# Performance work log

Hardware: AMD Instinct MI355X
Metric: run time of the kernel (lower is better)

## Reference

```python
import jax, jax.numpy as jnp
import numpy as np
from jax import lax

B, T, D, V, K = 32, 2048, 512, 1024, 3
COVERAGE_FLOOR = 0.05
LN_EPS = 1e-5


def _gelu(x):
    return jax.nn.gelu(x, approximate=False)  # torch F.gelu default is exact erf


def _causal_conv(h, w, b):
    # h: [B,T,D]; w: [D_out, D_in, K]; left-pad (K-1) for causality
    x = jnp.transpose(h, (0, 2, 1))  # [B,D,T]
    y = lax.conv_general_dilated(x, w, window_strides=(1,),
                                 padding=[(w.shape[-1] - 1, 0)],
                                 dimension_numbers=("NCH", "OIH", "NCH"))
    return jnp.transpose(y + b[None, :, None], (0, 2, 1))  # [B,T,D]


def _layer_norm(x, g, b):
    m = x.mean(-1, keepdims=True)
    v = ((x - m) ** 2).mean(-1, keepdims=True)
    return (x - m) / jnp.sqrt(v + LN_EPS) * g + b


def _masked_median(values, mask):
    # values, mask: [B,T]; torch median = lower middle = sorted[(n-1)//2]
    valid = mask > 0.5
    n = valid.sum(axis=1)  # [B]
    s = jnp.sort(jnp.where(valid, values, jnp.inf), axis=1)
    idx = jnp.clip((n - 1) // 2, 0, values.shape[1] - 1)
    med = jnp.take_along_axis(s, idx[:, None], axis=1)  # [B,1]
    return jnp.where((n > 0)[:, None], med, 0.0)


def _masked_mean(values, mask):
    denom = jnp.clip(mask.sum(axis=1, keepdims=True), 1.0, None)  # [B,1]
    return (values * mask[:, :, None]).sum(axis=1) / denom  # [B,D]


def _masked_std(values, mask, mean):
    denom = jnp.clip(mask.sum(axis=1, keepdims=True), 1.0, None)
    diff2 = (values - mean[:, None, :]) ** 2 * mask[:, :, None]
    return jnp.sqrt(diff2.sum(axis=1) / jnp.clip(denom, 1e-6, None) + 1e-6)


def setup_inputs() -> dict:
    key = jax.random.key(0)
    ks = jax.random.split(key, 16)
    s = 0.02
    return {
        "unit_ids": jax.random.randint(ks[0], (B, T), 0, V),
        "duration_obs": jax.random.uniform(ks[1], (B, T), jnp.float32, 0.01, 2.0),
        "mask": (jax.random.uniform(ks[2], (B, T)) > 0.3).astype(jnp.float32),
        "emb": jax.random.normal(ks[3], (V, D), jnp.float32) * s,
        "aux_w": jax.random.normal(ks[4], (D, 1), jnp.float32) * s,
        "aux_b": jnp.zeros((D,), jnp.float32),
        "conv1_w": jax.random.normal(ks[5], (D, D, K), jnp.float32) * s,
        "conv1_b": jnp.zeros((D,), jnp.float32),
        "conv2_w": jax.random.normal(ks[6], (D, D, K), jnp.float32) * s,
        "conv2_b": jnp.zeros((D,), jnp.float32),
        "ln_g": jnp.ones((D,), jnp.float32),
        "ln_b": jnp.zeros((D,), jnp.float32),
        "p1_w": jax.random.normal(ks[7], (D, 2 * D), jnp.float32) * s,
        "p1_b": jnp.zeros((D,), jnp.float32),
        "p2_w": jax.random.normal(ks[8], (D, D), jnp.float32) * s,
        "p2_b": jnp.zeros((D,), jnp.float32),
    }


def reference(unit_ids, duration_obs, mask, emb, aux_w, aux_b,
              conv1_w, conv1_b, conv2_w, conv2_b, ln_g, ln_b,
              p1_w, p1_b, p2_w, p2_b):
    mask = jnp.clip(mask.astype(jnp.float32), 0.0, 1.0)  # [B,T]
    logdur = jnp.log(jnp.clip(duration_obs.astype(jnp.float32), 1e-4, None)) * mask
    global_rate = _masked_median(logdur, mask)  # [B,1]
    ref_residual = (logdur - global_rate) * mask  # [B,T]

    # CausalStretchQueryEncoder
    hidden = emb[unit_ids] + (ref_residual[:, :, None] * aux_w[None, None, :, 0] + aux_b)
    hidden = _gelu(_causal_conv(hidden, conv1_w, conv1_b))
    hidden = _gelu(_causal_conv(hidden, conv2_w, conv2_b))
    hidden = _layer_norm(hidden, ln_g, ln_b) * mask[:, :, None]  # [B,T,D]

    mean = _masked_mean(hidden, mask)  # [B,D]
    std = _masked_std(hidden, mask, mean)  # [B,D]
    h = jnp.concatenate([mean, std], axis=-1)  # [B,2D]
    summary_state = jnp.tanh(_gelu(h @ p1_w.T + p1_b) @ p2_w.T + p2_b)  # [B,D]

    support_raw = mask.sum(axis=1, keepdims=True)  # [B,1]
    support = jnp.clip(support_raw, 1.0, None)
    summary_state = jnp.where(support_raw > 0.0, summary_state, 0.0)
    coverage = jnp.clip(support_raw / float(T), COVERAGE_FLOOR, None)

    residual_mean = (ref_residual * mask).sum(axis=1, keepdims=True) / support  # [B,1]
    residual_var = jnp.clip(((ref_residual - residual_mean) ** 2 * mask).sum(axis=1, keepdims=True) / support, 1e-4, None)
    attn = (mask / support)[:, :, None]  # [B,T,1]
    prompt_role_fit = residual_mean * jnp.ones_like(ref_residual) * mask  # [B,T]
    coeff_norm = jnp.linalg.norm(summary_state, axis=-1, keepdims=True)  # [B,1]

    return (global_rate, summary_state, residual_mean, residual_var, coverage,
            mask, logdur, ref_residual, attn, prompt_role_fit, coeff_norm)
```

## Files before the change

### kernel.cpp

```cpp
#include <hip/hip_runtime.h>
#include <hip/hip_bf16.h>
#include <math.h>

#define B_  32
#define T_  2048
#define D_  512
#define V_  1024
#define K_  3

typedef __attribute__((ext_vector_type(8))) short   short8;
typedef __attribute__((ext_vector_type(4))) float   floatx4;
typedef __attribute__((ext_vector_type(2))) long    longx2;

#define SCALE_H0 256.0f
#define SCALE_A  64.0f
#define SCALE_W  16.0f
#define INV1 (1.0f/(SCALE_H0*SCALE_W))
#define INV2 (1.0f/(SCALE_A*SCALE_W))

#define OFF0 0
#define OFF1 32
#define OFF2 16416
#define OFF3 16448
#define OFF4 16480
#define OFF5 16512
#define OFF6 82048
#define OFF7 147584
#define OFF8 213120
#define OFF9 278656
#define OFF10 344192

#define WS_RR     0
#define WS_SUP    262144
#define WS_PSUM   262272
#define WS_PSUMSQ 327808
#define WS_W1P    393344
#define WS_W2P    1212544
#define WS_H1     2031744
#define WS_S1     35618944
#define WS_NRM    35684480

__device__ __forceinline__ float clampf(float v, float lo, float hi) {
    v = (v > lo) ? v : lo;
    return (v < hi) ? v : hi;
}
__device__ __forceinline__ float gelu_exact(float v) {
    return 0.5f * v * (1.0f + erff(v * 0.70710678118654752440f));
}
__device__ __forceinline__ unsigned char f2fp8(float x) {
    int v = __builtin_amdgcn_cvt_pk_fp8_f32(x, x, 0, false);
    return (unsigned char)(v & 0xFF);
}
__device__ __forceinline__ int pk4fp8(float a, float b, float c, float d) {
    int p0 = __builtin_amdgcn_cvt_pk_fp8_f32(a, b, 0, false);
    int p1 = __builtin_amdgcn_cvt_pk_fp8_f32(c, d, 0, false);
    return (p1 << 16) | (p0 & 0xFFFF);
}

__device__ __forceinline__ float block_reduce_sum(float v, float* red, int tid) {
    __syncthreads();
    red[tid] = v;
    __syncthreads();
    for (int s = 128; s > 0; s >>= 1) {
        if (tid < s) red[tid] += red[tid + s];
        __syncthreads();
    }
    float r = red[0];
    __syncthreads();
    return r;
}

#define NB 2048
#define HLO (-9.3f)
#define HSC ((float)NB / 10.05f)
#define WLS 1544
__global__ __launch_bounds__(256) void init_kernel(
    const float* __restrict__ dur, const float* __restrict__ maskp,
    const float* __restrict__ w1, const float* __restrict__ w2,
    unsigned char* __restrict__ W1p, unsigned char* __restrict__ W2p,
    unsigned char* __restrict__ H1buf,
    float* __restrict__ rr_ws, float* __restrict__ sup_ws,
    float* __restrict__ psum, float* __restrict__ out)
{
    int tid = threadIdx.x;

    if (blockIdx.x >= 32) {
        __shared__ unsigned char Wl[2 * 16 * WLS];
        int ntg = blockIdx.x - 32;
        int lane = tid & 63, wave = tid >> 6;

        #pragma unroll
        for (int ws = 0; ws < 2; ++ws) {
            const float* wsrc = (ws ? w2 : w1) + (size_t)ntg * 16 * 1536;
            for (int i = tid; i < 6144; i += 256) {
                float4 v = ((const float4*)wsrc)[i];
                int col_local = i / 384;
                int pos = (i % 384) * 4;
                int word = pk4fp8(v.x * SCALE_W, v.y * SCALE_W,
                                  v.z * SCALE_W, v.w * SCALE_W);
                *(int*)(&Wl[(ws * 16 + col_local) * WLS + pos]) = word;
            }
        }
        __syncthreads();

        int cl = lane & 15, qq = lane >> 4;
        int pg = ntg >> 1, half = ntg & 1;
        #pragma unroll
        for (int ws = 0; ws < 2; ++ws) {
            unsigned char* dst = ws ? W2p : W1p;
            for (int s = wave; s < 48; s += 4) {
                int ci = s & 15, k = s >> 4;
                const unsigned char* row = &Wl[(ws * 16 + cl) * WLS];
                int kin = ci * 32 + qq * 8;
                unsigned char bb[8];
                #pragma unroll
                for (int e = 0; e < 8; ++e)
                    bb[e] = row[(kin + e) * 3 + k];
                *(double*)(dst + (((size_t)(s * 16 + pg) * 64 + lane) * 16
                                  + half * 8)) = *(double*)bb;
            }
        }

        int pid2 = ntg * 256 + tid;
        #pragma unroll
        for (int j = 0; j < 4; ++j) {
            int idx = pid2 + j * 8192;
            psum[idx] = 0.0f;
            int b = idx >> 10;
            int r = (idx >> 9) & 1;
            int d = idx & 511;
            H1buf[((size_t)b * 2050 + r) * 512 + d] = 0;
        }
        return;
    }

    __shared__ int   hist[NB];
    __shared__ int   csum[256];
    __shared__ float red[256];
    __shared__ float cand[128];
    __shared__ float nsh, medsh;
    __shared__ int   sh_tb, sh_cb, sh_candn;

    int b = blockIdx.x;
    const float* durb = dur + (size_t)b * T_;
    const float* mkb  = maskp + (size_t)b * T_;

    float ld[8], mk[8];
    int   bn[8];
    float cnt = 0.0f;
    #pragma unroll
    for (int i = 0; i < 8; ++i) hist[tid * 8 + i] = 0;
    __syncthreads();
    #pragma unroll
    for (int i = 0; i < 8; ++i) {
        int t = tid + i * 256;
        float m = clampf(mkb[t], 0.0f, 1.0f);
        float dv = durb[t];
        dv = (dv >= 1e-4f) ? dv : 1e-4f;
        float l = logf(dv) * m;
        ld[i] = l; mk[i] = m;
        int bin = (int)((l - HLO) * HSC);
        bin = (bin < 0) ? 0 : ((bin > NB - 1) ? NB - 1 : bin);
        bn[i] = bin;
        if (m > 0.5f) { cnt += 1.0f; atomicAdd(&hist[bin], 1); }
    }
    float n = block_reduce_sum(cnt, red, tid);
    if (tid == 0) { nsh = n; sh_candn = 0; medsh = 0.0f; }

    {
        int cs = 0;
        #pragma unroll
        for (int i = 0; i < 8; ++i) cs += hist[tid * 8 + i];
        csum[tid] = cs;
        __syncthreads();
        for (int off = 1; off < 256; off <<= 1) {
            int v = (tid >= off) ? csum[tid - off] : 0;
            __syncthreads();
            csum[tid] += v;
            __syncthreads();
        }
    }
    int ni = (int)(n + 0.5f);
    int k  = (ni > 0) ? ((ni - 1) >> 1) : 0;
    {
        int prevIncl = (tid > 0) ? csum[tid - 1] : 0;
        if (ni > 0 && k >= prevIncl && k < csum[tid]) {
            int cum = prevIncl, tb = tid * 8;
            #pragma unroll
            for (int i = 0; i < 8; ++i) {
                int c = hist[tid * 8 + i];
                if (k < cum + c) { tb = tid * 8 + i; break; }
                cum += c;
            }
            sh_tb = tb; sh_cb = cum;
        }
    }
    __syncthreads();
    if (ni > 0) {
        int tb = sh_tb;
        #pragma unroll
        for (int i = 0; i < 8; ++i) {
            if (mk[i] > 0.5f && bn[i] == tb) {
                int p = atomicAdd(&sh_candn, 1);
                if (p < 128) cand[p] = ld[i];
            }
        }
    }
    __syncthreads();
    if (tid == 0 && ni > 0) {
        int m = k - sh_cb;
        int cn = (sh_candn < 128) ? sh_candn : 128;
        float best = cand[0];
        for (int i = 0; i < cn; ++i) {
            int rank = 0;
            for (int j = 0; j < cn; ++j)
                rank += (cand[j] < cand[i]) || (cand[j] == cand[i] && j < i);
            if (rank == m) { best = cand[i]; break; }
        }
        medsh = best;
    }
    __syncthreads();
    float med = (ni > 0) ? medsh : 0.0f;
    med = clampf(med, -20.0f, 20.0f);

    float denom = (n > 1.0f) ? n : 1.0f;
    float rv[8];
    float ssum = 0.0f;
    #pragma unroll
    for (int i = 0; i < 8; ++i) { rv[i] = (ld[i] - med) * mk[i]; ssum += rv[i]; }
    float rsum = block_reduce_sum(ssum, red, tid);
    float rm = clampf(rsum / denom, -40.0f, 40.0f);

    float vsum_l = 0.0f;
    #pragma unroll
    for (int i = 0; i < 8; ++i) { float dd = rv[i] - rm; vsum_l += dd * dd * mk[i]; }
    float vsum = block_reduce_sum(vsum_l, red, tid);
    float var = clampf(vsum / denom, 1e-4f, 1e4f);

    float inv_sup = 1.0f / denom;
    #pragma unroll
    for (int i = 0; i < 8; ++i) {
        int t = tid + i * 256;
        size_t o = (size_t)b * T_ + t;
        out[OFF5 + o] = mk[i];
        out[OFF6 + o] = ld[i];
        out[OFF7 + o] = rv[i];
        out[OFF8 + o] = mk[i] * inv_sup;
        out[OFF9 + o] = rm * mk[i];
        rr_ws[o] = rv[i];
    }
    if (tid == 0) {
        out[OFF0 + b] = med;
        out[OFF2 + b] = rm;
        out[OFF3 + b] = var;
        float cov = n * (1.0f / (float)T_);
        out[OFF4 + b] = (cov > 0.05f) ? cov : 0.05f;
        sup_ws[b] = n;
    }
}

#define H0S 520
__global__ __launch_bounds__(256, 3) void conv1g_kernel(
    const int* __restrict__ ids, const float* __restrict__ rr,
    const float* __restrict__ emb,
    const float* __restrict__ aux_w, const float* __restrict__ aux_b,
    const unsigned char* __restrict__ W1p, const float* __restrict__ bias1,
    unsigned char* __restrict__ H1buf)
{
    __shared__ __align__(16) unsigned char H0s[66 * H0S];
    __shared__ int   lid[66];
    __shared__ float lrr[66];

    int tile = blockIdx.x;
    int b    = blockIdx.y;
    int r0   = tile << 6;
    int tid  = threadIdx.x;
    int wave = tid >> 6, lane = tid & 63;
    int q = lane >> 4, m16 = lane & 15;

    if (tid < 66) {
        int t = r0 - 2 + tid;
        bool v = (t >= 0);
        lid[tid] = v ? ids[b * T_ + t] : -1;
        lrr[tid] = v ? rr[(size_t)b * T_ + t] : 0.0f;
    }
    __syncthreads();

    {
        int c4 = tid & 127;
        float4 aw = *(const float4*)(aux_w + c4 * 4);
        float4 ab = *(const float4*)(aux_b + c4 * 4);
        int rbase = tid >> 7;
        for (int j = 0; j < 33; ++j) {
            int row = rbase + j * 2;
            int id = lid[row];
            int word = 0;
            if (id >= 0) {
                float vr = lrr[row];
                float4 e = *(const float4*)(emb + (size_t)id * D_ + c4 * 4);
                word = pk4fp8((e.x + vr * aw.x + ab.x) * SCALE_H0,
                              (e.y + vr * aw.y + ab.y) * SCALE_H0,
                              (e.z + vr * aw.z + ab.z) * SCALE_H0,
                              (e.w + vr * aw.w + ab.w) * SCALE_H0);
            }
            *(int*)(&H0s[row * H0S + c4 * 4]) = word;
        }
    }
    __syncthreads();

    unsigned char* Ob = H1buf + ((size_t)b * 2050 + 2 + r0) * 512;

#define CONV1_PHASE(FR0, FR1, SS)                                              \
    {   int k1 = (SS) >> 4, ci = (SS) & 15;                                    \
        _Pragma("unroll")                                                      \
        for (int mt = 0; mt < 4; ++mt) {                                       \
            long afr = *(const long*)(&H0s[(mt * 16 + m16 + k1) * H0S + ci * 32 + q * 8]); \
            acc[mt][0] = __builtin_amdgcn_mfma_f32_16x16x32_fp8_fp8(afr, FR0[0], acc[mt][0], 0, 0, 0); \
            acc[mt][1] = __builtin_amdgcn_mfma_f32_16x16x32_fp8_fp8(afr, FR0[1], acc[mt][1], 0, 0, 0); \
            acc[mt][2] = __builtin_amdgcn_mfma_f32_16x16x32_fp8_fp8(afr, FR1[0], acc[mt][2], 0, 0, 0); \
            acc[mt][3] = __builtin_amdgcn_mfma_f32_16x16x32_fp8_fp8(afr, FR1[1], acc[mt][3], 0, 0, 0); \
        } }

    #pragma unroll
    for (int nh = 0; nh < 2; ++nh) {
        floatx4 acc[4][4];
        #pragma unroll
        for (int i = 0; i < 4; ++i)
            #pragma unroll
            for (int j = 0; j < 4; ++j)
                acc[i][j] = (floatx4){0.f, 0.f, 0.f, 0.f};

        const longx2* wp0 = (const longx2*)W1p
                          + ((size_t)(0 * 16 + nh * 8 + wave * 2 + 0) * 64 + lane);
        const longx2* wp1 = wp0 + 64;

        longx2 fA0 = wp0[0],                  fA1 = wp1[0];
        longx2 fB0 = wp0[(size_t)1 * 1024],   fB1 = wp1[(size_t)1 * 1024];
        longx2 fC0, fC1, fD0, fD1;

        #pragma unroll 1
        for (int s = 0; s < 48; s += 4) {
            fC0 = wp0[(size_t)(s + 2) * 1024]; fC1 = wp1[(size_t)(s + 2) * 1024];
            CONV1_PHASE(fA0, fA1, s)
            fD0 = wp0[(size_t)(s + 3) * 1024]; fD1 = wp1[(size_t)(s + 3) * 1024];
            CONV1_PHASE(fB0, fB1, s + 1)
            fA0 = wp0[(size_t)(s + 4) * 1024]; fA1 = wp1[(size_t)(s + 4) * 1024];
            CONV1_PHASE(fC0, fC1, s + 2)
            fB0 = wp0[(size_t)(s + 5) * 1024]; fB1 = wp1[(size_t)(s + 5) * 1024];
            CONV1_PHASE(fD0, fD1, s + 3)
        }

        #pragma unroll
        for (int mt = 0; mt < 4; ++mt) {
            #pragma unroll
            for (int nt = 0; nt < 4; ++nt) {
                int col = nh * 256 + wave * 64 + nt * 16 + m16;
                float bsv = bias1[col];
                #pragma unroll
                for (int r = 0; r < 4; ++r) {
                    int row = mt * 16 + q * 4 + r;
                    float v = gelu_exact(acc[mt][nt][r] * INV1 + bsv) * SCALE_A;
                    Ob[(size_t)row * 512 + col] = f2fp8(v);
                }
            }
        }
    }
#undef CONV1_PHASE
}

#define H1S 520
__global__ __launch_bounds__(512, 2) void conv2ln_kernel(
    const unsigned char* __restrict__ H1buf, const unsigned char* __restrict__ W2p,
    const float* __restrict__ bias2,
    const float* __restrict__ ln_g, const float* __restrict__ ln_b,
    const float* __restrict__ maskp,
    float* __restrict__ psum, float* __restrict__ psumsq)
{
    __shared__ __align__(16) unsigned char H1s[66 * H1S];
    __shared__ __align__(16) unsigned char Wb[2][16384];
    __shared__ float mrow[64];
    __shared__ float part[64][4][2];
    __shared__ float tot[64][2];
    __shared__ float colsum[2][512][2];

    int tile = blockIdx.x;
    int b    = blockIdx.y;
    int r0   = tile << 6;
    int tid  = threadIdx.x;
    int wave = tid >> 6, lane = tid & 63;
    int mhalf = wave >> 2, nq = wave & 3;
    int q = lane >> 4, m16 = lane & 15;
    int nbase = nq << 7;

    const unsigned char* src = H1buf + ((size_t)b * 2050 + r0) * 512;
    for (int g = tid; g < 66 * 32; g += 512) {
        int row = g >> 5, h = g & 31;
        *(float4*)(&H1s[row * H1S + h * 16]) = *(const float4*)(src + (size_t)row * 512 + h * 16);
    }
    if (tid < 64)
        mrow[tid] = clampf(maskp[(size_t)b * T_ + r0 + tid], 0.0f, 1.0f);

    {
        const longx2* g0 = (const longx2*)W2p + tid;
        longx2 v0 = g0[0], v1 = g0[512];
        *(longx2*)(&Wb[0][tid * 16]) = v0;
        *(longx2*)(&Wb[0][tid * 16 + 8192]) = v1;
    }
    __syncthreads();

    floatx4 acc[2][8];
    #pragma unroll
    for (int i = 0; i < 2; ++i)
        #pragma unroll
        for (int j = 0; j < 8; ++j)
            acc[i][j] = (floatx4){0.f, 0.f, 0.f, 0.f};

#define C2_STEP(RB, WB_, SS)                                                   \
    {   const longx2* gq = (const longx2*)(W2p + (size_t)((SS) + 1) * 16384) + tid; \
        longx2 sv0 = gq[0];                                                    \
        longx2 sv1 = gq[512];                                                  \
        int k2 = (SS) >> 4, ci = (SS) & 15;                                    \
        longx2 f2[4];                                                          \
        _Pragma("unroll")                                                      \
        for (int ntp = 0; ntp < 4; ++ntp)                                      \
            f2[ntp] = *(const longx2*)(&RB[((nq * 4 + ntp) * 64 + lane) * 16]); \
        _Pragma("unroll")                                                      \
        for (int mt = 0; mt < 2; ++mt) {                                       \
            long afr = *(const long*)(&H1s[(mhalf * 32 + mt * 16 + m16 + k2) * H1S + ci * 32 + q * 8]); \
            _Pragma("unroll")                                                  \
            for (int ntp = 0; ntp < 4; ++ntp) {                                \
                acc[mt][2 * ntp]     = __builtin_amdgcn_mfma_f32_16x16x32_fp8_fp8( \
                    afr, f2[ntp][0], acc[mt][2 * ntp], 0, 0, 0);               \
                acc[mt][2 * ntp + 1] = __builtin_amdgcn_mfma_f32_16x16x32_fp8_fp8( \
                    afr, f2[ntp][1], acc[mt][2 * ntp + 1], 0, 0, 0);           \
            }                                                                  \
        }                                                                      \
        *(longx2*)(&WB_[tid * 16]) = sv0;                                      \
        *(longx2*)(&WB_[tid * 16 + 8192]) = sv1;                               \
        __syncthreads();                                                       \
    }

    #pragma unroll 1
    for (int s = 0; s < 48; s += 2) {
        C2_STEP(Wb[0], Wb[1], s)
        C2_STEP(Wb[1], Wb[0], s + 1)
    }
#undef C2_STEP

    #pragma unroll
    for (int mt = 0; mt < 2; ++mt)
        #pragma unroll
        for (int nt = 0; nt < 8; ++nt) {
            int col = nbase + nt * 16 + m16;
            float bsv = bias2[col];
            #pragma unroll
            for (int r = 0; r < 4; ++r)
                acc[mt][nt][r] = gelu_exact(acc[mt][nt][r] * INV2 + bsv);
        }

    #pragma unroll
    for (int mt = 0; mt < 2; ++mt) {
        #pragma unroll
        for (int r = 0; r < 4; ++r) {
            float rs = 0.f, rq = 0.f;
            #pragma unroll
            for (int nt = 0; nt < 8; ++nt) {
                float v = acc[mt][nt][r];
                rs += v; rq += v * v;
            }
            rs += __shfl_xor(rs, 1);  rq += __shfl_xor(rq, 1);
            rs += __shfl_xor(rs, 2);  rq += __shfl_xor(rq, 2);
            rs += __shfl_xor(rs, 4);  rq += __shfl_xor(rq, 4);
            rs += __shfl_xor(rs, 8);  rq += __shfl_xor(rq, 8);
            if (m16 == 0) {
                int row = mhalf * 32 + mt * 16 + q * 4 + r;
                part[row][nq][0] = rs;
                part[row][nq][1] = rq;
            }
        }
    }
    __syncthreads();
    if (tid < 128) {
        int row = tid >> 1, j = tid & 1;
        tot[row][j] = part[row][0][j] + part[row][1][j] + part[row][2][j] + part[row][3][j];
    }
    __syncthreads();

    float meanv[2][4], rstdv[2][4];
    #pragma unroll
    for (int mt = 0; mt < 2; ++mt)
        #pragma unroll
        for (int r = 0; r < 4; ++r) {
            int row = mhalf * 32 + mt * 16 + q * 4 + r;
            float m = tot[row][0] * (1.0f / D_);
            float var = tot[row][1] * (1.0f / D_) - m * m;
            meanv[mt][r] = m;
            rstdv[mt][r] = rsqrtf((var > 0.0f ? var : 0.0f) + 1e-5f);
        }

    float cs[8], cq[8];
    #pragma unroll
    for (int nt = 0; nt < 8; ++nt) { cs[nt] = 0.f; cq[nt] = 0.f; }
    #pragma unroll
    for (int mt = 0; mt < 2; ++mt) {
        #pragma unroll
        for (int r = 0; r < 4; ++r) {
            int row = mhalf * 32 + mt * 16 + q * 4 + r;
            float mk = mrow[row];
            float m = meanv[mt][r], rs = rstdv[mt][r];
            #pragma unroll
            for (int nt = 0; nt < 8; ++nt) {
                int col = nbase + nt * 16 + m16;
                float xn = ((acc[mt][nt][r] - m) * rs * ln_g[col] + ln_b[col]) * mk;
                cs[nt] += xn;
                cq[nt] += xn * xn;
            }
        }
    }
    #pragma unroll
    for (int nt = 0; nt < 8; ++nt) {
        cs[nt] += __shfl_xor(cs[nt], 16);  cq[nt] += __shfl_xor(cq[nt], 16);
        cs[nt] += __shfl_xor(cs[nt], 32);  cq[nt] += __shfl_xor(cq[nt], 32);
    }
    if (lane < 16) {
        #pragma unroll
        for (int nt = 0; nt < 8; ++nt) {
            int col = nbase + nt * 16 + m16;
            colsum[mhalf][col][0] = cs[nt];
            colsum[mhalf][col][1] = cq[nt];
        }
    }
    __syncthreads();
    {
        int i = tid;
        if (i < 512) {
            atomicAdd(&psum[(size_t)b * D_ + i],   colsum[0][i][0] + colsum[1][i][0]);
            atomicAdd(&psumsq[(size_t)b * D_ + i], colsum[0][i][1] + colsum[1][i][1]);
        }
    }
}

__global__ __launch_bounds__(128) void mlp1_kernel(
    const float* __restrict__ psum, const float* __restrict__ psumsq,
    const float* __restrict__ sup_ws,
    const float* __restrict__ p1w, const float* __restrict__ p1b,
    float* __restrict__ s1_ws, float* __restrict__ nrm_ws)
{
    int b = blockIdx.x, jt = blockIdx.y;
    int tid = threadIdx.x;
    __shared__ float h[2 * D_];

    float n = sup_ws[b];
    float denom = (n > 1.0f) ? n : 1.0f;
    for (int i = tid; i < D_; i += 128) {
        float S = psum[(size_t)b * D_ + i];
        float Q = psumsq[(size_t)b * D_ + i];
        float mean = S / denom;
        float msum = Q - 2.0f * mean * S + n * mean * mean;
        float arg = msum / denom + 1e-6f;
        h[i] = mean;
        h[D_ + i] = sqrtf((arg > 0.0f) ? arg : 0.0f);
    }
    if (jt == 0 && tid == 0) nrm_ws[b] = 0.0f;
    __syncthreads();

    int d  = jt * 64 + (tid >> 1);
    int kh = tid & 1;
    float z = (kh == 0) ? p1b[d] : 0.0f;
    const float4* w4 = (const float4*)(p1w + (size_t)d * (2 * D_) + kh * D_);
    const float*  hh = &h[kh * D_];
    for (int jj = 0; jj < D_ / 4; ++jj) {
        float4 wv = w4[jj];
        z += hh[jj * 4 + 0] * wv.x + hh[jj * 4 + 1] * wv.y
           + hh[jj * 4 + 2] * wv.z + hh[jj * 4 + 3] * wv.w;
    }
    z += __shfl_xor(z, 1);
    if (kh == 0) s1_ws[(size_t)b * D_ + d] = gelu_exact(z);
}

__global__ __launch_bounds__(128) void mlp2_kernel(
    const float* __restrict__ s1_ws, const float* __restrict__ sup_ws,
    const float* __restrict__ p2w, const float* __restrict__ p2b,
    float* __restrict__ nrm_ws, float* __restrict__ out)
{
    int b = blockIdx.x, jt = blockIdx.y;
    int tid = threadIdx.x;
    __shared__ float s1[D_];
    __shared__ float red[128];

    for (int i = tid; i < D_; i += 128) s1[i] = s1_ws[(size_t)b * D_ + i];
    __syncthreads();

    int d  = jt * 64 + (tid >> 1);
    int kh = tid & 1;
    float z2 = (kh == 0) ? p2b[d] : 0.0f;
    const float4* w24 = (const float4*)(p2w + (size_t)d * D_ + kh * 256);
    const float*  ss  = &s1[kh * 256];
    for (int jj = 0; jj < 64; ++jj) {
        float4 wv = w24[jj];
        z2 += ss[jj * 4 + 0] * wv.x + ss[jj * 4 + 1] * wv.y
            + ss[jj * 4 + 2] * wv.z + ss[jj * 4 + 3] * wv.w;
    }
    z2 += __shfl_xor(z2, 1);
    float nsup = sup_ws[b];
    float st = tanhf(z2);
    if (!(nsup > 0.0f)) st = 0.0f;
    if (kh == 0) out[OFF1 + (size_t)b * D_ + d] = st;

    red[tid] = (kh == 0) ? st * st : 0.0f;
    __syncthreads();
    for (int s = 64; s > 0; s >>= 1) {
        if (tid < s) red[tid] += red[tid + s];
        __syncthreads();
    }
    if (tid == 0) atomicAdd(&nrm_ws[b], red[0]);
}

__global__ __launch_bounds__(64) void mlp3_kernel(
    const float* __restrict__ nrm_ws, float* __restrict__ out)
{
    int b = threadIdx.x;
    if (b < B_) out[OFF10 + b] = sqrtf(nrm_ws[b]);
}

extern "C" void kernel_launch(void* const* d_in, const int* in_sizes, int n_in,
                              void* d_out, int out_size, void* d_ws, size_t ws_size,
                              hipStream_t stream) {
    (void)in_sizes; (void)n_in; (void)out_size; (void)ws_size;
    const int*   unit_ids = (const int*)d_in[0];
    const float* dur      = (const float*)d_in[1];
    const float* mask     = (const float*)d_in[2];
    const float* emb      = (const float*)d_in[3];
    const float* aux_w    = (const float*)d_in[4];
    const float* aux_b    = (const float*)d_in[5];
    const float* conv1_w  = (const float*)d_in[6];
    const float* conv1_b  = (const float*)d_in[7];
    const float* conv2_w  = (const float*)d_in[8];
    const float* conv2_b  = (const float*)d_in[9];
    const float* ln_g     = (const float*)d_in[10];
    const float* ln_b     = (const float*)d_in[11];
    const float* p1_w     = (const float*)d_in[12];
    const float* p1_b     = (const float*)d_in[13];
    const float* p2_w     = (const float*)d_in[14];
    const float* p2_b     = (const float*)d_in[15];
    float* out = (float*)d_out;

    char* ws = (char*)d_ws;
    float*          rr     = (float*)(ws + WS_RR);
    float*          sup    = (float*)(ws + WS_SUP);
    float*          psum   = (float*)(ws + WS_PSUM);
    float*          psumsq = (float*)(ws + WS_PSUMSQ);
    unsigned char*  W1p    = (unsigned char*)(ws + WS_W1P);
    unsigned char*  W2p    = (unsigned char*)(ws + WS_W2P);
    unsigned char*  H1buf  = (unsigned char*)(ws + WS_H1);
    float*          s1_ws  = (float*)(ws + WS_S1);
    float*          nrm_ws = (float*)(ws + WS_NRM);

    init_kernel<<<dim3(64), dim3(256), 0, stream>>>(
        dur, mask, conv1_w, conv2_w, W1p, W2p, H1buf, rr, sup, psum, out);
    conv1g_kernel<<<dim3(32, 32), dim3(256), 0, stream>>>(
        unit_ids, rr, emb, aux_w, aux_b, W1p, conv1_b, H1buf);
    conv2ln_kernel<<<dim3(32, 32), dim3(512), 0, stream>>>(
        H1buf, W2p, conv2_b, ln_g, ln_b, mask, psum, psumsq);
    mlp1_kernel<<<dim3(32, 8), dim3(128), 0, stream>>>(
        psum, psumsq, sup, p1_w, p1_b, s1_ws, nrm_ws);
    mlp2_kernel<<<dim3(32, 8), dim3(128), 0, stream>>>(
        s1_ws, sup, p2_w, p2_b, nrm_ws, out);
    mlp3_kernel<<<dim3(1), dim3(64), 0, stream>>>(nrm_ws, out);
}
```

Measured before the change: 342.8 us.

## Load conv2 weight fragments directly to registers and drop LDS weight staging

The conv2+LayerNorm kernel now runs 4 waves of 256 threads instead of 8 waves of 512. Each wave covers all 64 rows and 128 output columns, split across two 256-column halves. Weight fragments are loaded from global memory straight into registers, software-pipelined two steps ahead, instead of being staged through a double-buffered LDS buffer with a block barrier every K-step. This removes 48 __syncthreads and the LDS weight traffic, but doubles the accumulator registers per thread and halves the threads per block, which may cost occupancy and latency hiding.

Result: slower. 519.9 us (+51.7%).

```diff
diff --git a/kernel.cpp b/kernel.cpp
--- a/kernel.cpp
+++ b/kernel.cpp
@@ -369,7 +369,7 @@
 }
 
 #define H1S 520
-__global__ __launch_bounds__(512, 2) void conv2ln_kernel(
+__global__ __launch_bounds__(256, 2) void conv2ln_kernel(
     const unsigned char* __restrict__ H1buf, const unsigned char* __restrict__ W2p,
     const float* __restrict__ bias2,
     const float* __restrict__ ln_g, const float* __restrict__ ln_b,
@@ -377,105 +377,110 @@
     float* __restrict__ psum, float* __restrict__ psumsq)
 {
     __shared__ __align__(16) unsigned char H1s[66 * H1S];
-    __shared__ __align__(16) unsigned char Wb[2][16384];
     __shared__ float mrow[64];
     __shared__ float part[64][4][2];
     __shared__ float tot[64][2];
-    __shared__ float colsum[2][512][2];
+    __shared__ float colsum[512][2];
 
     int tile = blockIdx.x;
     int b    = blockIdx.y;
     int r0   = tile << 6;
     int tid  = threadIdx.x;
     int wave = tid >> 6, lane = tid & 63;
-    int mhalf = wave >> 2, nq = wave & 3;
     int q = lane >> 4, m16 = lane & 15;
-    int nbase = nq << 7;
 
     const unsigned char* src = H1buf + ((size_t)b * 2050 + r0) * 512;
-    for (int g = tid; g < 66 * 32; g += 512) {
+    for (int g = tid; g < 66 * 32; g += 256) {
         int row = g >> 5, h = g & 31;
         *(float4*)(&H1s[row * H1S + h * 16]) = *(const float4*)(src + (size_t)row * 512 + h * 16);
     }
     if (tid < 64)
         mrow[tid] = clampf(maskp[(size_t)b * T_ + r0 + tid], 0.0f, 1.0f);
-
-    {
-        const longx2* g0 = (const longx2*)W2p + tid;
-        longx2 v0 = g0[0], v1 = g0[512];
-        *(longx2*)(&Wb[0][tid * 16]) = v0;
-        *(longx2*)(&Wb[0][tid * 16 + 8192]) = v1;
-    }
-    __syncthreads();
-
-    floatx4 acc[2][8];
-    #pragma unroll
-    for (int i = 0; i < 2; ++i)
-        #pragma unroll
-        for (int j = 0; j < 8; ++j)
-            acc[i][j] = (floatx4){0.f, 0.f, 0.f, 0.f};
-
-#define C2_STEP(RB, WB_, SS)                                                   \
-    {   const longx2* gq = (const longx2*)(W2p + (size_t)((SS) + 1) * 16384) + tid; \
-        longx2 sv0 = gq[0];                                                    \
-        longx2 sv1 = gq[512];                                                  \
-        int k2 = (SS) >> 4, ci = (SS) & 15;                                    \
-        longx2 f2[4];                                                          \
+    __syncthreads();
+
+    floatx4 accA[4][4], accB[4][4];
+    #pragma unroll
+    for (int i = 0; i < 4; ++i)
+        #pragma unroll
+        for (int j = 0; j < 4; ++j) {
+            accA[i][j] = (floatx4){0.f, 0.f, 0.f, 0.f};
+            accB[i][j] = (floatx4){0.f, 0.f, 0.f, 0.f};
+        }
+
+    const longx2* wp0 = (const longx2*)W2p + ((size_t)(wave * 2) * 64 + lane);
+    const longx2* wp1 = wp0 + 64;
+    const longx2* wp2 = (const longx2*)W2p + ((size_t)(8 + wave * 2) * 64 + lane);
+    const longx2* wp3 = wp2 + 64;
+
+#define C2_PHASE(F0, F1, F2, F3, SS)                                           \
+    {   int k2 = (SS) >> 4, ci = (SS) & 15;                                    \
         _Pragma("unroll")                                                      \
-        for (int ntp = 0; ntp < 4; ++ntp)                                      \
-            f2[ntp] = *(const longx2*)(&RB[((nq * 4 + ntp) * 64 + lane) * 16]); \
-        _Pragma("unroll")                                                      \
-        for (int mt = 0; mt < 2; ++mt) {                                       \
-            long afr = *(const long*)(&H1s[(mhalf * 32 + mt * 16 + m16 + k2) * H1S + ci * 32 + q * 8]); \
-            _Pragma("unroll")                                                  \
-            for (int ntp = 0; ntp < 4; ++ntp) {                                \
-                acc[mt][2 * ntp]     = __builtin_amdgcn_mfma_f32_16x16x32_fp8_fp8( \
-                    afr, f2[ntp][0], acc[mt][2 * ntp], 0, 0, 0);               \
-                acc[mt][2 * ntp + 1] = __builtin_amdgcn_mfma_f32_16x16x32_fp8_fp8( \
-                    afr, f2[ntp][1], acc[mt][2 * ntp + 1], 0, 0, 0);           \
-            }                                                                  \
-        }                                                                      \
-        *(longx2*)(&WB_[tid * 16]) = sv0;                                      \
-        *(longx2*)(&WB_[tid * 16 + 8192]) = sv1;                               \
-        __syncthreads();                                                       \
-    }
+        for (int mt = 0; mt < 4; ++mt) {                                       \
+            long afr = *(const long*)(&H1s[(mt * 16 + m16 + k2) * H1S + ci * 32 + q * 8]); \
+            accA[mt][0] = __builtin_amdgcn_mfma_f32_16x16x32_fp8_fp8(afr, F0[0], accA[mt][0], 0, 0, 0); \
+            accA[mt][1] = __builtin_amdgcn_mfma_f32_16x16x32_fp8_fp8(afr, F0[1], accA[mt][1], 0, 0, 0); \
+            accA[mt][2] = __builtin_amdgcn_mfma_f32_16x16x32_fp8_fp8(afr, F1[0], accA[mt][2], 0, 0, 0); \
+            accA[mt][3] = __builtin_amdgcn_mfma_f32_16x16x32_fp8_fp8(afr, F1[1], accA[mt][3], 0, 0, 0); \
+            accB[mt][0] = __builtin_amdgcn_mfma_f32_16x16x32_fp8_fp8(afr, F2[0], accB[mt][0], 0, 0, 0); \
+            accB[mt][1] = __builtin_amdgcn_mfma_f32_16x16x32_fp8_fp8(afr, F2[1], accB[mt][1], 0, 0, 0); \
+            accB[mt][2] = __builtin_amdgcn_mfma_f32_16x16x32_fp8_fp8(afr, F3[0], accB[mt][2], 0, 0, 0); \
+            accB[mt][3] = __builtin_amdgcn_mfma_f32_16x16x32_fp8_fp8(afr, F3[1], accB[mt][3], 0, 0, 0); \
+        } }
+
+    longx2 fA0 = wp0[0], fA1 = wp1[0], fA2 = wp2[0], fA3 = wp3[0];
+    longx2 fB0 = wp0[(size_t)1 * 1024], fB1 = wp1[(size_t)1 * 1024];
+    longx2 fB2 = wp2[(size_t)1 * 1024], fB3 = wp3[(size_t)1 * 1024];
+    longx2 fC0, fC1, fC2, fC3, fD0, fD1, fD2, fD3;
 
     #pragma unroll 1
-    for (int s = 0; s < 48; s += 2) {
-        C2_STEP(Wb[0], Wb[1], s)
-        C2_STEP(Wb[1], Wb[0], s + 1)
-    }
-#undef C2_STEP
-
-    #pragma unroll
-    for (int mt = 0; mt < 2; ++mt)
-        #pragma unroll
-        for (int nt = 0; nt < 8; ++nt) {
-            int col = nbase + nt * 16 + m16;
-            float bsv = bias2[col];
+    for (int s = 0; s < 48; s += 4) {
+        fC0 = wp0[(size_t)(s + 2) * 1024]; fC1 = wp1[(size_t)(s + 2) * 1024];
+        fC2 = wp2[(size_t)(s + 2) * 1024]; fC3 = wp3[(size_t)(s + 2) * 1024];
+        C2_PHASE(fA0, fA1, fA2, fA3, s)
+        fD0 = wp0[(size_t)(s + 3) * 1024]; fD1 = wp1[(size_t)(s + 3) * 1024];
+        fD2 = wp2[(size_t)(s + 3) * 1024]; fD3 = wp3[(size_t)(s + 3) * 1024];
+        C2_PHASE(fB0, fB1, fB2, fB3, s + 1)
+        fA0 = wp0[(size_t)(s + 4) * 1024]; fA1 = wp1[(size_t)(s + 4) * 1024];
+        fA2 = wp2[(size_t)(s + 4) * 1024]; fA3 = wp3[(size_t)(s + 4) * 1024];
+        C2_PHASE(fC0, fC1, fC2, fC3, s + 2)
+        fB0 = wp0[(size_t)(s + 5) * 1024]; fB1 = wp1[(size_t)(s + 5) * 1024];
+        fB2 = wp2[(size_t)(s + 5) * 1024]; fB3 = wp3[(size_t)(s + 5) * 1024];
+        C2_PHASE(fD0, fD1, fD2, fD3, s + 3)
+    }
+#undef C2_PHASE
+
+    #pragma unroll
+    for (int mt = 0; mt < 4; ++mt)
+        #pragma unroll
+        for (int nt = 0; nt < 4; ++nt) {
+            int colA = wave * 64 + nt * 16 + m16;
+            float bA = bias2[colA];
+            float bB = bias2[colA + 256];
             #pragma unroll
-            for (int r = 0; r < 4; ++r)
-                acc[mt][nt][r] = gelu_exact(acc[mt][nt][r] * INV2 + bsv);
-        }
-
-    #pragma unroll
-    for (int mt = 0; mt < 2; ++mt) {
+            for (int r = 0; r < 4; ++r) {
+                accA[mt][nt][r] = gelu_exact(accA[mt][nt][r] * INV2 + bA);
+                accB[mt][nt][r] = gelu_exact(accB[mt][nt][r] * INV2 + bB);
+            }
+        }
+
+    #pragma unroll
+    for (int mt = 0; mt < 4; ++mt) {
         #pragma unroll
         for (int r = 0; r < 4; ++r) {
             float rs = 0.f, rq = 0.f;
             #pragma unroll
-            for (int nt = 0; nt < 8; ++nt) {
-                float v = acc[mt][nt][r];
-                rs += v; rq += v * v;
+            for (int nt = 0; nt < 4; ++nt) {
+                float vA = accA[mt][nt][r], vB = accB[mt][nt][r];
+                rs += vA + vB; rq += vA * vA + vB * vB;
             }
             rs += __shfl_xor(rs, 1);  rq += __shfl_xor(rq, 1);
             rs += __shfl_xor(rs, 2);  rq += __shfl_xor(rq, 2);
             rs += __shfl_xor(rs, 4);  rq += __shfl_xor(rq, 4);
             rs += __shfl_xor(rs, 8);  rq += __shfl_xor(rq, 8);
             if (m16 == 0) {
-                int row = mhalf * 32 + mt * 16 + q * 4 + r;
-                part[row][nq][0] = rs;
-                part[row][nq][1] = rq;
+                int row = mt * 16 + q * 4 + r;
+                part[row][wave][0] = rs;
+                part[row][wave][1] = rq;
             }
         }
     }
@@ -486,57 +491,62 @@
     }
     __syncthreads();
 
-    float meanv[2][4], rstdv[2][4];
-    #pragma unroll
-    for (int mt = 0; mt < 2; ++mt)
+    float meanv[4][4], rstdv[4][4];
+    #pragma unroll
+    for (int mt = 0; mt < 4; ++mt)
         #pragma unroll
         for (int r = 0; r < 4; ++r) {
-            int row = mhalf * 32 + mt * 16 + q * 4 + r;
+            int row = mt * 16 + q * 4 + r;
             float m = tot[row][0] * (1.0f / D_);
             float var = tot[row][1] * (1.0f / D_) - m * m;
             meanv[mt][r] = m;
             rstdv[mt][r] = rsqrtf((var > 0.0f ? var : 0.0f) + 1e-5f);
         }
 
-    float cs[8], cq[8];
-    #pragma unroll
-    for (int nt = 0; nt < 8; ++nt) { cs[nt] = 0.f; cq[nt] = 0.f; }
-    #pragma unroll
-    for (int mt = 0; mt < 2; ++mt) {
+    float csA[4], cqA[4], csB[4], cqB[4];
+    float lgA[4], lbA[4], lgB[4], lbB[4];
+    #pragma unroll
+    for (int nt = 0; nt < 4; ++nt) {
+        int colA = wave * 64 + nt * 16 + m16;
+        lgA[nt] = ln_g[colA];       lbA[nt] = ln_b[colA];
+        lgB[nt] = ln_g[colA + 256]; lbB[nt] = ln_b[colA + 256];
+        csA[nt] = 0.f; cqA[nt] = 0.f; csB[nt] = 0.f; cqB[nt] = 0.f;
+    }
+    #pragma unroll
+    for (int mt = 0; mt < 4; ++mt) {
         #pragma unroll
         for (int r = 0; r < 4; ++r) {
-            int row = mhalf * 32 + mt * 16 + q * 4 + r;
+            int row = mt * 16 + q * 4 + r;
             float mk = mrow[row];
             float m = meanv[mt][r], rs = rstdv[mt][r];
             #pragma unroll
-            for (int nt = 0; nt < 8; ++nt) {
-                int col = nbase + nt * 16 + m16;
-                float xn = ((acc[mt][nt][r] - m) * rs * ln_g[col] + ln_b[col]) * mk;
-                cs[nt] += xn;
-                cq[nt] += xn * xn;
-            }
-        }
-    }
-    #pragma unroll
-    for (int nt = 0; nt < 8; ++nt) {
-        cs[nt] += __shfl_xor(cs[nt], 16);  cq[nt] += __shfl_xor(cq[nt], 16);
-        cs[nt] += __shfl_xor(cs[nt], 32);  cq[nt] += __shfl_xor(cq[nt], 32);
+            for (int nt = 0; nt < 4; ++nt) {
+                float xnA = ((accA[mt][nt][r] - m) * rs * lgA[nt] + lbA[nt]) * mk;
+                float xnB = ((accB[mt][nt][r] - m) * rs * lgB[nt] + lbB[nt]) * mk;
+                csA[nt] += xnA; cqA[nt] += xnA * xnA;
+                csB[nt] += xnB; cqB[nt] += xnB * xnB;
+            }
+        }
+    }
+    #pragma unroll
+    for (int nt = 0; nt < 4; ++nt) {
+        csA[nt] += __shfl_xor(csA[nt], 16);  cqA[nt] += __shfl_xor(cqA[nt], 16);
+        csA[nt] += __shfl_xor(csA[nt], 32);  cqA[nt] += __shfl_xor(cqA[nt], 32);
+        csB[nt] += __shfl_xor(csB[nt], 16);  cqB[nt] += __shfl_xor(cqB[nt], 16);
+        csB[nt] += __shfl_xor(csB[nt], 32);  cqB[nt] += __shfl_xor(cqB[nt], 32);
     }
     if (lane < 16) {
         #pragma unroll
-        for (int nt = 0; nt < 8; ++nt) {
-            int col = nbase + nt * 16 + m16;
-            colsum[mhalf][col][0] = cs[nt];
-            colsum[mhalf][col][1] = cq[nt];
-        }
-    }
-    __syncthreads();
-    {
-        int i = tid;
-        if (i < 512) {
-            atomicAdd(&psum[(size_t)b * D_ + i],   colsum[0][i][0] + colsum[1][i][0]);
-            atomicAdd(&psumsq[(size_t)b * D_ + i], colsum[0][i][1] + colsum[1][i][1]);
-        }
+        for (int nt = 0; nt < 4; ++nt) {
+            int colA = wave * 64 + nt * 16 + m16;
+            colsum[colA][0] = csA[nt];       colsum[colA][1] = cqA[nt];
+            colsum[colA + 256][0] = csB[nt]; colsum[colA + 256][1] = cqB[nt];
+        }
+    }
+    __syncthreads();
+    for (int i = tid; i < 512; i += 256) {
+        atomicAdd(&psum[(size_t)b * D_ + i], colsum[i][0]);
+        atomicAdd(&psumsq[(size_t)b * D_ + i], colsum[i][1]);
     }
 }
 
@@ -660,7 +670,7 @@
         dur, mask, conv1_w, conv2_w, W1p, W2p, H1buf, rr, sup, psum, out);
     conv1g_kernel<<<dim3(32, 32), dim3(256), 0, stream>>>(
         unit_ids, rr, emb, aux_w, aux_b, W1p, conv1_b, H1buf);
-    conv2ln_kernel<<<dim3(32, 32), dim3(512), 0, stream>>>(
+    conv2ln_kernel<<<dim3(32, 32), dim3(256), 0, stream>>>(
         H1buf, W2p, conv2_b, ln_g, ln_b, mask, psum, psumsq);
     mlp1_kernel<<<dim3(32, 8), dim3(128), 0, stream>>>(
         psum, psumsq, sup, p1_w, p1_b, s1_ws, nrm_ws);
```
